# Performance work log

Measured on AMD Instinct MI355X. Metric: run time of the kernel, lower is better.

## Reference

```python
import jax, jax.numpy as jnp
import numpy as np

B, L, DM, E, N, R, S = 2, 1024, 512, 1024, 16, 32, 64
BN_SCALE = float(1.0 / np.sqrt(1.0 + 1e-5))  # eval-mode BatchNorm1d with default running stats


def _ssm(x, Wx, bx, Wdt, bdt, A_log, D):
    # x: [B,L,E] -> Mamba selective scan output [B,L,E]
    dbc = x @ Wx.T + bx                                   # [B,L,R+2N]
    delta = jax.nn.softplus(dbc[..., :R] @ Wdt.T + bdt)   # [B,L,E]
    Bm = dbc[..., R:R + N]                                # [B,L,N]
    Cm = dbc[..., R + N:]                                 # [B,L,N]
    A = -jnp.exp(A_log)                                   # [E,N]
    dA = jnp.exp(delta[..., None] * A)                    # [B,L,E,N]
    dBx = delta[..., None] * Bm[:, :, None, :] * x[..., None]

    def comb(c1, c2):
        a1, b1 = c1
        a2, b2 = c2
        return a1 * a2, b1 * a2 + b2

    _, h = jax.lax.associative_scan(comb, (dA, dBx), axis=1)  # [B,L,E,N]
    return jnp.einsum('blen,bln->ble', h, Cm) + D * x


def _gmask_idx(length, batch):
    ref = (length + 1) // 2
    idx = jnp.arange(length, dtype=jnp.float32)
    sigma = jnp.abs(idx - ref).mean()
    w = jnp.exp(-0.5 * (idx - ref) ** 2 / sigma ** 2)
    w = w / w.sum()
    return jnp.broadcast_to(w, (batch, length))


def _gmask_vec(seq):
    length = seq.shape[1]
    ref = seq[:, (length + 1) // 2, :]
    d = jnp.linalg.norm(seq - ref[:, None, :], axis=2)    # [B,L]
    sigma = d.mean(axis=1, keepdims=True)
    w = jnp.exp(-0.5 * (d / sigma) ** 2)
    return w / w.sum(axis=1, keepdims=True)


def _spatial_attn(x, w, b):
    # x: [B,L,C]; SpatialAttention: returns weighted map in [B,C,L] layout
    xt = jnp.swapaxes(x, 1, 2)                            # [B,C,L]
    fmap = (w[0] * xt.max(axis=1) + w[1] * xt.mean(axis=1) + b) * BN_SCALE
    wmap = jax.nn.sigmoid(jax.nn.relu(fmap))[:, None, :]  # [B,1,L]
    return xt * wmap                                      # [B,C,L]


def _forward(x, W_in_x, b_in_x, W_in_z, b_in_z, convf_w, convf_b, convb_w, convb_b,
             Wx_f, bx_f, Wdt_f, bdt_f, A_log_f, D_f,
             Wx_b, bx_b, Wdt_b, bdt_b, A_log_b, D_b,
             W_cat, b_cat, sa_w, sa_b, wA_f, wV_f,
             W_proj, b_proj, W_Bi, b_Bi, tf_w, tf_b, W_out, b_out):
    b_, l_, _ = x.shape
    xi = x @ W_in_x.T + b_in_x                            # [B,L,E]
    z = x @ W_in_z.T + b_in_z                             # [B,L,E]
    # depthwise conv1d with kernel_size=1 == per-channel affine
    x_f = jax.nn.silu(xi * convf_w + convf_b)
    x_b = jax.nn.silu(jnp.flip(xi, axis=1) * convb_w + convb_b)
    y_f = jnp.tanh(_ssm(x_f, Wx_f, bx_f, Wdt_f, bdt_f, A_log_f, D_f))
    y_b = jnp.tanh(_ssm(x_b, Wx_b, bx_b, Wdt_b, bdt_b, A_log_b, D_b))
    gi = _gmask_idx(l_, b_)
    mf = jax.nn.softmax(gi * _gmask_vec(y_f), axis=1)
    mb = jax.nn.softmax(gi * _gmask_vec(y_b), axis=1)
    y_cat = jnp.concatenate([y_f * mf[..., None],
                             y_b * jnp.flip(mb[..., None], axis=1)], axis=-1)
    y = y_cat @ W_cat.T + b_cat                           # [B,L,E]
    m = jax.nn.softmax(gi * _gmask_vec(y_cat), axis=1)
    y = y * m[..., None]
    yw = _spatial_attn(y, sa_w, sa_b)                     # [B,E,L]
    y = jnp.swapaxes(yw, 1, 2)                            # [B,L,E]
    # STL tokenizer (forward direction weights)
    Aw = jax.nn.softmax(jnp.swapaxes(y @ wA_f.T, 1, 2), axis=-1)  # [B,S,L]
    u = Aw @ (y @ wV_f)                                   # [B,S,E]
    # z branch: adaptive average pool L -> S (L % S == 0), then SiLU
    zp = jax.nn.silu(jnp.swapaxes(z, 1, 2).reshape(b_, E, S, l_ // S).mean(-1))
    zt = jnp.swapaxes(zp, 1, 2)                           # [B,S,E]
    # TokenFuser -- faithful to original's .view-based memory reinterpretation
    Y = (u.reshape(b_, E, S) @ W_proj.T + b_proj).reshape(b_, S, E)
    Bw = jax.nn.sigmoid(zt @ W_Bi.T + b_Bi)               # [B,S,S]
    BwY = Bw @ Y                                          # [B,S,E]
    xj = _spatial_attn(zt, tf_w, tf_b).reshape(b_, S, E)  # view (reshape), not transpose
    out = BwY + xj
    return jnp.tanh(out @ W_out.T + b_out)                # [B,S,DM]


def setup_inputs():
    ks = jax.random.split(jax.random.key(0), 24)
    g = lambda i, shape, s=0.02: jax.random.normal(ks[i], shape, dtype=jnp.float32) * s
    A_log = jnp.log(jnp.tile(jnp.arange(1, N + 1, dtype=jnp.float32), (E, 1)))
    return dict(
        x=jax.random.normal(ks[0], (B, L, DM), dtype=jnp.float32),
        W_in_x=g(1, (E, DM)), b_in_x=jnp.zeros((E,), jnp.float32),
        W_in_z=g(2, (E, DM)), b_in_z=jnp.zeros((E,), jnp.float32),
        convf_w=1.0 + g(3, (E,)), convf_b=jnp.zeros((E,), jnp.float32),
        convb_w=1.0 + g(4, (E,)), convb_b=jnp.zeros((E,), jnp.float32),
        Wx_f=g(5, (R + 2 * N, E)), bx_f=jnp.zeros((R + 2 * N,), jnp.float32),
        Wdt_f=g(6, (E, R)), bdt_f=jnp.full((E,), -4.0, jnp.float32),
        A_log_f=A_log, D_f=jnp.ones((E,), jnp.float32),
        Wx_b=g(7, (R + 2 * N, E)), bx_b=jnp.zeros((R + 2 * N,), jnp.float32),
        Wdt_b=g(8, (E, R)), bdt_b=jnp.full((E,), -4.0, jnp.float32),
        A_log_b=A_log, D_b=jnp.ones((E,), jnp.float32),
        W_cat=g(9, (E, 2 * E)), b_cat=jnp.zeros((E,), jnp.float32),
        sa_w=g(10, (2,), 0.5), sa_b=jnp.zeros((), jnp.float32),
        wA_f=g(11, (S, E), 0.05), wV_f=g(12, (E, E), 0.02),
        W_proj=g(13, (S, S), 0.1), b_proj=jnp.zeros((S,), jnp.float32),
        W_Bi=g(14, (S, E)), b_Bi=jnp.zeros((S,), jnp.float32),
        tf_w=g(15, (2,), 0.5), tf_b=jnp.zeros((), jnp.float32),
        W_out=g(16, (DM, E)), b_out=jnp.zeros((DM,), jnp.float32),
    )


def reference(x, W_in_x, b_in_x, W_in_z, b_in_z, convf_w, convf_b, convb_w, convb_b,
              Wx_f, bx_f, Wdt_f, bdt_f, A_log_f, D_f,
              Wx_b, bx_b, Wdt_b, bdt_b, A_log_b, D_b,
              W_cat, b_cat, sa_w, sa_b, wA_f, wV_f,
              W_proj, b_proj, W_Bi, b_Bi, tf_w, tf_b, W_out, b_out):
    return _forward(x, W_in_x, b_in_x, W_in_z, b_in_z, convf_w, convf_b, convb_w, convb_b,
                    Wx_f, bx_f, Wdt_f, bdt_f, A_log_f, D_f,
                    Wx_b, bx_b, Wdt_b, bdt_b, A_log_b, D_b,
                    W_cat, b_cat, sa_w, sa_b, wA_f, wV_f,
                    W_proj, b_proj, W_Bi, b_Bi, tf_w, tf_b, W_out, b_out)
```

## Files before the change

kernel.cpp:

```cpp
#include <hip/hip_runtime.h>
#include <math.h>

#define DEVI static __device__ __forceinline__

namespace {

constexpr float BN_SCALE_C = 0.9999950000374997f;

typedef __bf16 bf8v __attribute__((ext_vector_type(8)));
typedef float f4v __attribute__((ext_vector_type(4)));

DEVI float sigmoidf_(float x){ return 1.0f/(1.0f+expf(-x)); }
DEVI float siluf_(float x){ return x/(1.0f+expf(-x)); }
DEVI float softplusf_(float x){ return fmaxf(x,0.0f) + log1pf(__expf(-fabsf(x))); }

DEVI unsigned short f2bf(float f){
  union{float f; unsigned int u;} v; v.f=f;
  unsigned int r = v.u + 0x7fffu + ((v.u>>16)&1u);
  return (unsigned short)(r>>16);
}

DEVI float bredw_sum(float v, float* sh){
  #pragma unroll
  for (int o=32;o;o>>=1) v += __shfl_xor(v, o);
  __syncthreads();
  if ((threadIdx.x&63)==0) sh[threadIdx.x>>6] = v;
  __syncthreads();
  return sh[0]+sh[1]+sh[2]+sh[3];
}
DEVI float bredw_max(float v, float* sh){
  #pragma unroll
  for (int o=32;o;o>>=1) v = fmaxf(v, __shfl_xor(v, o));
  __syncthreads();
  if ((threadIdx.x&63)==0) sh[threadIdx.x>>6] = v;
  __syncthreads();
  return fmaxf(fmaxf(sh[0],sh[1]), fmaxf(sh[2],sh[3]));
}

DEVI void gld_lds16(const unsigned short* g, unsigned short* l){
  __builtin_amdgcn_global_load_lds(
      (const __attribute__((address_space(1))) unsigned int*)(g),
      (__attribute__((address_space(3))) unsigned int*)(l), 16, 0, 0);
}

DEVI void stage_tile64(const unsigned short* __restrict__ Ak,
                       const unsigned short* __restrict__ Bk,
                       size_t lda, size_t ldb,
                       unsigned short* As, unsigned short* Bs,
                       int w, int lane)
{
  #pragma unroll
  for (int i=0;i<2;++i){
    int seg = (w<<1) + i;
    int row = (seg<<3) + (lane>>3);
    int c   = (lane & 7) ^ (row & 7);
    gld_lds16(Ak + (size_t)row*lda + (c<<3), As + (seg<<9));
    gld_lds16(Bk + (size_t)row*ldb + (c<<3), Bs + (seg<<9));
  }
}

DEVI void gemm_core(const unsigned short* __restrict__ Ag,
                    const unsigned short* __restrict__ Bg,
                    size_t lda, size_t ldb, int ksteps,
                    unsigned short* As, unsigned short* Bs, f4v (&acc)[2][2])
{
  const int tid = threadIdx.x;
  const int lane = tid & 63, w = tid >> 6;
  const int wr = w >> 1, wc = w & 1;
  const int l15 = lane & 15, l4 = lane >> 4;

  int cur = 0;
  stage_tile64(Ag, Bg, lda, ldb, As, Bs, w, lane);
  asm volatile("s_waitcnt vmcnt(0)" ::: "memory");
  __syncthreads();
  for (int ks = 0; ks < ksteps; ++ks){
    unsigned short* Asc = As + (cur<<12);
    unsigned short* Bsc = Bs + (cur<<12);
    if (ks+1 < ksteps)
      stage_tile64(Ag + (size_t)(ks+1)*64, Bg + (size_t)(ks+1)*64, lda, ldb,
                   As + ((cur^1)<<12), Bs + ((cur^1)<<12), w, lane);
    #pragma unroll
    for (int kk=0;kk<2;++kk){
      int cb = (kk<<2) + l4;
      bf8v af[2], bfv[2];
      #pragma unroll
      for (int mi=0;mi<2;++mi){
        int row = (wr<<5)+(mi<<4)+l15;
        af[mi] = *(const bf8v*)(Asc + (row<<6) + ((cb^(row&7))<<3));
      }
      #pragma unroll
      for (int ni=0;ni<2;++ni){
        int row = (wc<<5)+(ni<<4)+l15;
        bfv[ni] = *(const bf8v*)(Bsc + (row<<6) + ((cb^(row&7))<<3));
      }
      #pragma unroll
      for (int mi=0;mi<2;++mi)
        #pragma unroll
        for (int ni=0;ni<2;++ni)
          acc[mi][ni] = __builtin_amdgcn_mfma_f32_16x16x32_bf16(af[mi], bfv[ni], acc[mi][ni], 0,0,0);
    }
    asm volatile("s_waitcnt vmcnt(0)" ::: "memory");
    __syncthreads();
    cur ^= 1;
  }
}

template<int EPI>
__global__ __launch_bounds__(256) void gemm_bf16_k(
    const unsigned short* __restrict__ A, const unsigned short* __restrict__ Bt,
    const float* __restrict__ bias, void* __restrict__ Cout,
    int N, int K,
    const unsigned short* __restrict__ Bt2, const float* __restrict__ bias2, long sC)
{
  __shared__ unsigned short As[8192], Bs[8192];
  float* Cf = (float*)Cout;
  if (Bt2 && blockIdx.z){ Bt = Bt2; bias = bias2; Cf += sC; }
  const int m0 = blockIdx.y<<6, n0 = blockIdx.x<<6;
  f4v acc[2][2] = {};
  gemm_core(A + (size_t)m0*K, Bt + (size_t)n0*K, K, K, K>>6, As, Bs, acc);
  const int lane = threadIdx.x & 63, w = threadIdx.x >> 6;
  const int wr = w>>1, wc = w&1, l15 = lane&15, l4 = lane>>4;
  #pragma unroll
  for (int mi=0;mi<2;++mi)
    #pragma unroll
    for (int ni=0;ni<2;++ni){
      int col = n0 + (wc<<5) + (ni<<4) + l15;
      float bv = bias ? bias[col] : 0.f;
      #pragma unroll
      for (int r=0;r<4;++r){
        int rowg = m0 + (wr<<5) + (mi<<4) + (l4<<2) + r;
        Cf[(size_t)rowg*N + col] = acc[mi][ni][r] + bv;
      }
    }
}

template<int EPI>
__global__ __launch_bounds__(256) void gemm_small_k(
    const unsigned short* __restrict__ A, const unsigned short* __restrict__ Bt,
    const float* __restrict__ b0, const float* __restrict__ b1,
    void* __restrict__ Cout, int N, int K, int mshift, long sB)
{
  __shared__ unsigned char smem[65536];
  unsigned short* AsAll = (unsigned short*)smem;
  unsigned short* BsAll = (unsigned short*)(smem + 32768);
  float* Lc = (float*)smem;

  const int tid = threadIdx.x;
  const int lane = tid & 63, w = tid >> 6;
  const int m0 = blockIdx.y<<6, n0 = blockIdx.x<<6;
  const unsigned short* Ab = A + (size_t)m0*K;
  const unsigned short* Bb = Bt + (size_t)(m0>>mshift)*sB + (size_t)n0*K;
  unsigned short* Asw = AsAll + (w<<12);
  unsigned short* Bsw = BsAll + (w<<12);
  const int kpw = K >> 2;
  const int nst = kpw >> 6;
  const int l15 = lane & 15, l4 = lane >> 4;
  const int srow8 = lane >> 3, sc = lane & 7;

  f4v acc[4][4] = {};
  for (int ks = 0; ks < nst; ++ks){
    const int kbase = w*kpw + (ks<<6);
    #pragma unroll
    for (int seg=0; seg<8; ++seg){
      int row = (seg<<3) + srow8;
      int c = sc ^ (row & 7);
      gld_lds16(Ab + (size_t)row*K + kbase + (c<<3), Asw + (seg<<9));
      gld_lds16(Bb + (size_t)row*K + kbase + (c<<3), Bsw + (seg<<9));
    }
    asm volatile("s_waitcnt vmcnt(0)" ::: "memory");
    #pragma unroll
    for (int kk=0; kk<2; ++kk){
      int cb = (kk<<2) + l4;
      bf8v af[4], bfv[4];
      #pragma unroll
      for (int mi=0;mi<4;++mi){
        int row = (mi<<4) + l15;
        af[mi] = *(const bf8v*)(Asw + (row<<6) + ((cb^(row&7))<<3));
      }
      #pragma unroll
      for (int ni=0;ni<4;++ni){
        int row = (ni<<4) + l15;
        bfv[ni] = *(const bf8v*)(Bsw + (row<<6) + ((cb^(row&7))<<3));
      }
      #pragma unroll
      for (int mi=0;mi<4;++mi)
        #pragma unroll
        for (int ni=0;ni<4;++ni)
          acc[mi][ni] = __builtin_amdgcn_mfma_f32_16x16x32_bf16(af[mi], bfv[ni], acc[mi][ni], 0,0,0);
    }
    __builtin_amdgcn_sched_barrier(0);
  }
  __syncthreads();
  #pragma unroll
  for (int mi=0;mi<4;++mi)
    #pragma unroll
    for (int ni=0;ni<4;++ni){
      int col = (ni<<4) + l15;
      #pragma unroll
      for (int r=0;r<4;++r){
        int row = (mi<<4) + (l4<<2) + r;
        Lc[(w<<12) + (row<<6) + col] = acc[mi][ni][r];
      }
    }
  __syncthreads();
  {
    const int basei = tid << 4;
    const int row = basei >> 6, colb = basei & 63;
    float vals[16];
    #pragma unroll
    for (int q=0;q<4;++q){
      float4 a0 = *(const float4*)(Lc + basei + (q<<2));
      float4 a1 = *(const float4*)(Lc + 4096 + basei + (q<<2));
      float4 a2 = *(const float4*)(Lc + 8192 + basei + (q<<2));
      float4 a3 = *(const float4*)(Lc + 12288 + basei + (q<<2));
      vals[(q<<2)+0] = a0.x+a1.x+a2.x+a3.x;
      vals[(q<<2)+1] = a0.y+a1.y+a2.y+a3.y;
      vals[(q<<2)+2] = a0.z+a1.z+a2.z+a3.z;
      vals[(q<<2)+3] = a0.w+a1.w+a2.w+a3.w;
    }
    if (EPI==1){
      unsigned short* Cb = (unsigned short*)Cout + (size_t)(m0+row)*N + n0 + colb;
      union{unsigned short u[16]; uint4 q[2];} o;
      #pragma unroll
      for (int j=0;j<16;++j) o.u[j] = f2bf(vals[j]);
      *(uint4*)(Cb) = o.q[0];
      *(uint4*)(Cb+8) = o.q[1];
    } else {
      const float* bias = (b1 && (m0>>mshift)) ? b1 : b0;
      float* Cb = (float*)Cout + (size_t)(m0+row)*N + n0 + colb;
      #pragma unroll
      for (int q=0;q<4;++q){
        float4 v;
        float* vp = &v.x;
        #pragma unroll
        for (int j=0;j<4;++j){
          float t = vals[(q<<2)+j] + (bias ? bias[n0+colb+(q<<2)+j] : 0.f);
          if (EPI==2) t = tanhf(t);
          vp[j] = t;
        }
        *(float4*)(Cb + (q<<2)) = v;
      }
    }
  }
}

__global__ __launch_bounds__(256) void castall_k(
    const float* __restrict__ s0, unsigned short* __restrict__ d0, int n0,
    const float* __restrict__ s1, unsigned short* __restrict__ d1, int n1,
    const float* __restrict__ s2, unsigned short* __restrict__ d2, int n2,
    const float* __restrict__ s3, unsigned short* __restrict__ d3, int n3,
    const float* __restrict__ s4, unsigned short* __restrict__ d4, int n4,
    const float* __restrict__ s5, unsigned short* __restrict__ d5, int n5,
    const float* __restrict__ s6, unsigned short* __restrict__ d6, int n6,
    const float* __restrict__ s7, unsigned short* __restrict__ d7, int n7,
    const float* __restrict__ wV, unsigned short* __restrict__ wVT,
    const float* __restrict__ Wdt_f, const float* __restrict__ Wdt_b,
    float* __restrict__ WdtT)
{
  __shared__ float tsh[32][33];
  if (blockIdx.x >= 4800){
    int tb = blockIdx.x - 4800;
    int tx = threadIdx.x & 31, ty = threadIdx.x >> 5;
    if (tb < 1024){
      int by = tb >> 5, bx = tb & 31;
      #pragma unroll
      for (int r=0;r<4;++r){
        int row = by*32 + ty + r*8;
        tsh[ty + r*8][tx] = wV[(long)row*1024 + bx*32 + tx];
      }
      __syncthreads();
      #pragma unroll
      for (int r=0;r<4;++r){
        int row = bx*32 + ty + r*8;
        wVT[(long)row*1024 + by*32 + tx] = f2bf(tsh[tx][ty + r*8]);
      }
    } else {
      int q = tb - 1024;
      int dir = q >> 5, bi = q & 31;
      const float* src = dir ? Wdt_b : Wdt_f;
      float* dst = WdtT + (dir<<15);
      #pragma unroll
      for (int r=0;r<4;++r){
        int row = bi*32 + ty + r*8;
        tsh[ty + r*8][tx] = src[(long)row*32 + tx];
      }
      __syncthreads();
      #pragma unroll
      for (int r=0;r<4;++r){
        int c = ty + r*8;
        dst[(long)c*1024 + bi*32 + tx] = tsh[tx][c];
      }
    }
    return;
  }
  int i = (blockIdx.x*256 + threadIdx.x)*4;
  const float* s; unsigned short* d;
  if (i < n0){ s = s0; d = d0; }
  else if ((i -= n0) < n1){ s = s1; d = d1; }
  else if ((i -= n1) < n2){ s = s2; d = d2; }
  else if ((i -= n2) < n3){ s = s3; d = d3; }
  else if ((i -= n3) < n4){ s = s4; d = d4; }
  else if ((i -= n4) < n5){ s = s5; d = d5; }
  else if ((i -= n5) < n6){ s = s6; d = d6; }
  else if ((i -= n6) < n7){ s = s7; d = d7; }
  else return;
  float4 v = *(const float4*)(s + i);
  union{ unsigned short u[4]; uint2 p; } o;
  o.u[0]=f2bf(v.x); o.u[1]=f2bf(v.y); o.u[2]=f2bf(v.z); o.u[3]=f2bf(v.w);
  *(uint2*)(d + i) = o.p;
}

__global__ __launch_bounds__(256) void convzt_k(const float* __restrict__ xi, const float* __restrict__ z,
    const float* __restrict__ cfw, const float* __restrict__ cfb,
    const float* __restrict__ cbw, const float* __restrict__ cbb,
    float* __restrict__ xf, float* __restrict__ xb, unsigned short* __restrict__ xfb_bf,
    float* __restrict__ ztb)
{
  int bx = blockIdx.x, t = threadIdx.x;
  if (bx < 2048){
    int base = (bx*256 + t) << 2;
    int e = base & 1023;
    int bl = base >> 10; int l = bl & 1023, b = bl >> 10;
    float4 cw = *(const float4*)(cfw + e);
    float4 cb = *(const float4*)(cfb + e);
    float4 xv = *(const float4*)(xi + base);
    float4 vf;
    vf.x = siluf_(fmaf(xv.x, cw.x, cb.x));
    vf.y = siluf_(fmaf(xv.y, cw.y, cb.y));
    vf.z = siluf_(fmaf(xv.z, cw.z, cb.z));
    vf.w = siluf_(fmaf(xv.w, cw.w, cb.w));
    *(float4*)(xf + base) = vf;
    union{unsigned short u[4]; uint2 p;} o;
    o.u[0]=f2bf(vf.x); o.u[1]=f2bf(vf.y); o.u[2]=f2bf(vf.z); o.u[3]=f2bf(vf.w);
    *(uint2*)(xfb_bf + base) = o.p;
    int jb = (((b<<10) + (1023-l))<<10) + e;
    float4 cw2 = *(const float4*)(cbw + e);
    float4 cb2 = *(const float4*)(cbb + e);
    float4 xw = *(const float4*)(xi + jb);
    float4 vb;
    vb.x = siluf_(fmaf(xw.x, cw2.x, cb2.x));
    vb.y = siluf_(fmaf(xw.y, cw2.y, cb2.y));
    vb.z = siluf_(fmaf(xw.z, cw2.z, cb2.z));
    vb.w = siluf_(fmaf(xw.w, cw2.w, cb2.w));
    *(float4*)(xb + base) = vb;
    union{unsigned short u[4]; uint2 p;} o2;
    o2.u[0]=f2bf(vb.x); o2.u[1]=f2bf(vb.y); o2.u[2]=f2bf(vb.z); o2.u[3]=f2bf(vb.w);
    *(uint2*)(xfb_bf + 2097152 + base) = o2.p;
  } else {
    int base = ((bx-2048)*256 + t) << 2;
    int e = base & 1023; int bs = base >> 10; int s = bs & 63; int b = bs >> 6;
    const float* zp = z + (((long)((b<<10)+(s<<4)))<<10) + e;
    float4 sm = {0.f,0.f,0.f,0.f};
    #pragma unroll
    for (int j=0;j<16;++j){
      float4 v = *(const float4*)(zp + ((long)j<<10));
      sm.x += v.x; sm.y += v.y; sm.z += v.z; sm.w += v.w;
    }
    float4 o;
    o.x = siluf_(sm.x*(1.f/16.f)); o.y = siluf_(sm.y*(1.f/16.f));
    o.z = siluf_(sm.z*(1.f/16.f)); o.w = siluf_(sm.w*(1.f/16.f));
    *(float4*)(ztb + base) = o;
  }
}

__global__ __launch_bounds__(256) void ssm_chunk_k(
    const float* __restrict__ xs0, const float* __restrict__ dbc0,
    const float* __restrict__ A_log_f, const float* __restrict__ A_log_b,
    const float* __restrict__ WdtT,
    const float* __restrict__ bdt_f, const float* __restrict__ bdt_b,
    float* __restrict__ pA0, float* __restrict__ hend0)
{
  const int dir = blockIdx.y;
  const float* xs   = xs0  + (size_t)dir*2097152;
  const float* dbc  = dbc0 + (size_t)dir*131072;
  const float* A_log= dir ? A_log_b : A_log_f;
  float* pA   = pA0   + (size_t)dir*1048576;
  float* hend = hend0 + (size_t)dir*1048576;

  __shared__ float sB[32][16];
  __shared__ float sD[32][32];
  int g = blockIdx.x*256 + threadIdx.x;
  int e = g & 1023;
  int bc = g >> 10;
  int c = bc & 31, b = bc >> 5;
  for (int i=threadIdx.x; i<512; i+=256){
    int l=i>>4, n=i&15;
    sB[l][n] = dbc[(((b<<10) + (c<<5) + l)<<6) + 32 + n];
  }
  for (int i=threadIdx.x; i<1024; i+=256){
    int l=i>>5, k=i&31;
    sD[l][k] = dbc[(((b<<10) + (c<<5) + l)<<6) + k];
  }
  __syncthreads();
  float wdt[32];
  {
    const float* WT = WdtT + (dir<<15) + e;
    #pragma unroll
    for (int k=0;k<32;++k) wdt[k] = WT[(size_t)k<<10];
  }
  const float bde = (dir ? bdt_b : bdt_f)[e];
  float An[16];
  #pragma unroll
  for (int n=0;n<16;++n) An[n] = -__expf(A_log[(e<<4)+n]);
  float h[16], p[16];
  #pragma unroll
  for (int n=0;n<16;++n){ h[n]=0.0f; p[n]=1.0f; }
  long base = ((long)((b<<10) + (c<<5)))*1024 + e;
  for (int l=0;l<32;++l){
    float accd = bde;
    #pragma unroll
    for (int k=0;k<32;++k) accd = fmaf(sD[l][k], wdt[k], accd);
    float dl = softplusf_(accd);
    float xv = xs[base + ((long)l<<10)];
    float dx = dl*xv;
    #pragma unroll
    for (int n=0;n<16;++n){
      float a = __expf(dl*An[n]);
      h[n] = fmaf(a, h[n], dx*sB[l][n]);
      p[n] *= a;
    }
  }
  long ob = ((long)((b<<5)+c)<<4)*1024 + e;
  #pragma unroll
  for (int n=0;n<16;++n){ pA[ob + ((long)n<<10)] = p[n]; hend[ob + ((long)n<<10)] = h[n]; }
}

__global__ __launch_bounds__(256) void ssm_carry_k(
    const float* __restrict__ pA, const float* __restrict__ hend, float* __restrict__ Hc)
{
  int i = blockIdx.x*256 + threadIdx.x;
  int e = i & 1023, n = (i>>10)&15, b = (i>>14)&1, dir = (i>>15)&1;
  const float* pAd = pA   + (size_t)dir*1048576;
  const float* hd  = hend + (size_t)dir*1048576;
  float* Hd        = Hc   + (size_t)dir*1048576;
  float H = 0.f;
  long base = ((long)(b*512 + n))*1024 + e;
  for (int c=0;c<32;++c){
    long a = base + (long)c*16384;
    Hd[a] = H;
    H = fmaf(pAd[a], H, hd[a]);
  }
}

__global__ __launch_bounds__(256) void ssm_out_k(
    const float* __restrict__ xs0, const float* __restrict__ dbc0,
    const float* __restrict__ A_log_f, const float* __restrict__ A_log_b,
    const float* __restrict__ WdtT,
    const float* __restrict__ bdt_f, const float* __restrict__ bdt_b,
    const float* __restrict__ Hc0,
    const float* __restrict__ D_f, const float* __restrict__ D_b,
    float* __restrict__ y0)
{
  const int dir = blockIdx.y;
  const float* xs   = xs0  + (size_t)dir*2097152;
  const float* dbc  = dbc0 + (size_t)dir*131072;
  const float* A_log= dir ? A_log_b : A_log_f;
  const float* Hc   = Hc0 + (size_t)dir*1048576;
  const float* D    = dir ? D_b : D_f;
  float* y          = y0 + (size_t)dir*2097152;

  __shared__ float sB[32][16], sC[32][16];
  __shared__ float sD[32][32];
  int g = blockIdx.x*256+threadIdx.x;
  int e = g & 1023;
  int bc = g >> 10;
  int c = bc & 31, b = bc >> 5;
  for (int i=threadIdx.x;i<512;i+=256){
    int l=i>>4, n=i&15;
    int base = ((b<<10)+(c<<5)+l)<<6;
    sB[l][n] = dbc[base+32+n];
    sC[l][n] = dbc[base+48+n];
  }
  for (int i=threadIdx.x; i<1024; i+=256){
    int l=i>>5, k=i&31;
    sD[l][k] = dbc[(((b<<10) + (c<<5) + l)<<6) + k];
  }
  __syncthreads();
  float wdt[32];
  {
    const float* WT = WdtT + (dir<<15) + e;
    #pragma unroll
    for (int k=0;k<32;++k) wdt[k] = WT[(size_t)k<<10];
  }
  const float bde = (dir ? bdt_b : bdt_f)[e];
  float An[16], h[16];
  long ib = ((long)((b<<5)+c)<<4)*1024 + e;
  #pragma unroll
  for(int n=0;n<16;++n){ An[n] = -__expf(A_log[(e<<4)+n]); h[n]=Hc[ib+((long)n<<10)]; }
  float Dv = D[e];
  long base = ((long)((b<<10)+(c<<5)))*1024 + e;
  for (int l=0;l<32;++l){
    float accd = bde;
    #pragma unroll
    for (int k=0;k<32;++k) accd = fmaf(sD[l][k], wdt[k], accd);
    float dl = softplusf_(accd);
    float xv = xs[base+((long)l<<10)];
    float dx = dl*xv;
    float acc = Dv*xv;
    #pragma unroll
    for(int n=0;n<16;++n){
      float a = __expf(dl*An[n]);
      h[n] = fmaf(a,h[n],dx*sB[l][n]);
      acc = fmaf(h[n], sC[l][n], acc);
    }
    y[base+((long)l<<10)] = tanhf(acc);
  }
}

__global__ __launch_bounds__(256) void stats_k(const float* __restrict__ y,
    float* __restrict__ nrm, float* __restrict__ dotv)
{
  __shared__ float sh[4];
  int row = blockIdx.x;
  int rowref = (row & ~1023) + 512;
  const float4* rp  = (const float4*)(y + (long)row*1024);
  const float4* rf  = (const float4*)(y + (long)rowref*1024);
  float4 a = rp[threadIdx.x], r = rf[threadIdx.x];
  float sn = a.x*a.x + a.y*a.y + a.z*a.z + a.w*a.w;
  float sd = a.x*r.x + a.y*r.y + a.z*r.z + a.w*r.w;
  sn = bredw_sum(sn, sh);
  sd = bredw_sum(sd, sh);
  if (threadIdx.x==0){ nrm[row] = sn; dotv[row] = sd; }
}

DEVI void softmask(const float (&d)[4], const float (&gi)[4], float gsum,
                   float* sh, float (&m)[4])
{
  float s = d[0]+d[1]+d[2]+d[3];
  float sig = bredw_sum(s, sh) * (1.0f/1024.0f);
  float inv = 1.0f/sig;
  float w[4]; s = 0.f;
  #pragma unroll
  for (int i=0;i<4;++i){ float r = d[i]*inv; w[i] = __expf(-0.5f*r*r); s += w[i]; }
  float wsm = bredw_sum(s, sh);
  float sc = 1.0f/(wsm*gsum);
  float tv[4]; float mx = -1e30f;
  #pragma unroll
  for (int i=0;i<4;++i){ tv[i] = gi[i]*w[i]*sc; mx = fmaxf(mx, tv[i]); }
  mx = bredw_max(mx, sh);
  s = 0.f;
  #pragma unroll
  for (int i=0;i<4;++i){ tv[i] = __expf(tv[i]-mx); s += tv[i]; }
  float es = bredw_sum(s, sh);
  float ie = 1.0f/es;
  #pragma unroll
  for (int i=0;i<4;++i) m[i] = tv[i]*ie;
}

__global__ __launch_bounds__(256) void mask2_k(
    const float* __restrict__ nrm, const float* __restrict__ dotv,
    float* __restrict__ mfG, float* __restrict__ mbG, float* __restrict__ mvG)
{
  __shared__ float mfs[1024], mbs[1024], sh[4];
  const int b = blockIdx.x, t = threadIdx.x;
  const float nf512 = nrm[(b<<10)+512];
  const float nb512 = nrm[2048+(b<<10)+512];
  float gi[4], nf[4], pf[4], nb[4], pb[4];
  float gs = 0.f;
  #pragma unroll
  for (int i=0;i<4;++i){
    int l = t + (i<<8);
    float q = (float)(l-512) * (1.0f/256.0f);
    gi[i] = __expf(-0.5f*q*q); gs += gi[i];
    nf[i] = nrm[(b<<10)+l];      pf[i] = dotv[(b<<10)+l];
    nb[i] = nrm[2048+(b<<10)+l]; pb[i] = dotv[2048+(b<<10)+l];
  }
  float gsum = bredw_sum(gs, sh);
  float mf[4], mb[4], d[4];
  #pragma unroll
  for (int i=0;i<4;++i) d[i] = sqrtf(fmaxf(nf[i] - 2.f*pf[i] + nf512, 0.f));
  softmask(d, gi, gsum, sh, mf);
  #pragma unroll
  for (int i=0;i<4;++i) d[i] = sqrtf(fmaxf(nb[i] - 2.f*pb[i] + nb512, 0.f));
  softmask(d, gi, gsum, sh, mb);
  #pragma unroll
  for (int i=0;i<4;++i){
    int l = t + (i<<8);
    mfs[l] = mf[i]; mbs[l] = mb[i];
    mfG[(b<<10)+l] = mf[i]; mbG[(b<<10)+l] = mb[i];
  }
  __syncthreads();
  const float mf512 = mfs[512], mb511 = mbs[511];
  #pragma unroll
  for (int i=0;i<4;++i){
    int l = t + (i<<8);
    float mbf = mbs[1023-l];
    float dc2 = mf[i]*mf[i]*nf[i] - 2.f*mf[i]*mf512*pf[i] + mf512*mf512*nf512
              + mbf*mbf*nb[i]     - 2.f*mbf*mb511*pb[i]   + mb511*mb511*nb512;
    d[i] = sqrtf(fmaxf(dc2, 0.f));
  }
  float mv[4];
  softmask(d, gi, gsum, sh, mv);
  #pragma unroll
  for (int i=0;i<4;++i) mvG[(b<<10)+t+(i<<8)] = mv[i];
}

__global__ __launch_bounds__(256) void ycat_k(const float* __restrict__ yf, const float* __restrict__ yb,
    const float* __restrict__ mf, const float* __restrict__ mb, unsigned short* __restrict__ yc)
{
  int base = (blockIdx.x*256 + threadIdx.x) << 2;
  int e = base & 1023; int bl = base >> 10; int l = bl & 1023, b = bl >> 10;
  float mfv = mf[bl];
  float mbv = mb[(b<<10) + (1023-l)];
  float4 vf = *(const float4*)(yf + base);
  float4 vb = *(const float4*)(yb + base);
  long r = (long)bl*2048;
  union{unsigned short u[4]; uint2 p;} o;
  o.u[0]=f2bf(vf.x*mfv); o.u[1]=f2bf(vf.y*mfv); o.u[2]=f2bf(vf.z*mfv); o.u[3]=f2bf(vf.w*mfv);
  *(uint2*)(yc + r + e) = o.p;
  union{unsigned short u[4]; uint2 p;} o2;
  o2.u[0]=f2bf(vb.x*mbv); o2.u[1]=f2bf(vb.y*mbv); o2.u[2]=f2bf(vb.z*mbv); o2.u[3]=f2bf(vb.w*mbv);
  *(uint2*)(yc + r + 1024 + e) = o2.p;
}

__global__ __launch_bounds__(256) void rowscale_k(const float* __restrict__ y, const float* __restrict__ m,
    const float* __restrict__ sw, const float* __restrict__ sb, unsigned short* __restrict__ yo)
{
  __shared__ float sh[4];
  int row = blockIdx.x;
  float mv = m[row];
  float4 v = ((const float4*)(y + (long)row*1024))[threadIdx.x];
  v.x *= mv; v.y *= mv; v.z *= mv; v.w *= mv;
  float mx = fmaxf(fmaxf(v.x,v.y), fmaxf(v.z,v.w));
  float sm = v.x+v.y+v.z+v.w;
  float rmax = bredw_max(mx, sh);
  float rsum = bredw_sum(sm, sh);
  float fmap = (sw[0]*rmax + sw[1]*(rsum*(1.0f/1024.0f)) + sb[0])*BN_SCALE_C;
  float sc = sigmoidf_(fmaxf(fmap, 0.0f));
  union{unsigned short u[4]; uint2 p;} o;
  o.u[0]=f2bf(v.x*sc); o.u[1]=f2bf(v.y*sc); o.u[2]=f2bf(v.z*sc); o.u[3]=f2bf(v.w*sc);
  *(uint2*)(yo + (long)row*1024 + (threadIdx.x<<2)) = o.p;
}

__global__ __launch_bounds__(256) void awsmT_k(const float* __restrict__ yA,
    unsigned short* __restrict__ Aw,
    const unsigned short* __restrict__ src, unsigned short* __restrict__ dst)
{
  __shared__ float sh[4];
  __shared__ unsigned short tsh[32][33];
  if (blockIdx.x < 128){
    int bs = blockIdx.x; int b = bs >> 6, s = bs & 63;
    float v[4]; float mx=-1e30f;
    #pragma unroll
    for(int i=0;i<4;++i){
      int l = threadIdx.x+(i<<8);
      v[i] = yA[(long)((b<<10)+l)*64 + s];
      mx = fmaxf(mx, v[i]);
    }
    mx = bredw_max(mx, sh);
    float sm=0.0f;
    #pragma unroll
    for(int i=0;i<4;++i){ v[i]=__expf(v[i]-mx); sm+=v[i]; }
    sm = bredw_sum(sm, sh);
    float inv = 1.0f/sm;
    #pragma unroll
    for(int i=0;i<4;++i){ int l=threadIdx.x+(i<<8); Aw[(((b<<6)+s)<<10)+l] = f2bf(v[i]*inv); }
  } else {
    int tb = blockIdx.x - 128;
    size_t bo = (size_t)(tb>>10) << 20;
    int rem = tb & 1023;
    int by = rem >> 5, bx = rem & 31;
    int tx = threadIdx.x & 31, ty = threadIdx.x >> 5;
    #pragma unroll
    for (int r=0;r<4;++r){
      int row = by*32 + ty + r*8;
      tsh[ty + r*8][tx] = src[bo + (long)row*1024 + bx*32 + tx];
    }
    __syncthreads();
    #pragma unroll
    for (int r=0;r<4;++r){
      int row = bx*32 + ty + r*8;
      dst[bo + (long)row*1024 + by*32 + tx] = tsh[tx][ty + r*8];
    }
  }
}

__global__ __launch_bounds__(256) void upbw_k(const float* __restrict__ u2f,
    const float* __restrict__ W_proj, const float* __restrict__ b_proj,
    const float* __restrict__ zt, const float* __restrict__ W_Bi,
    const float* __restrict__ b_Bi, const float* __restrict__ tw,
    const float* __restrict__ tb,
    float* __restrict__ Yp, float* __restrict__ Bw, float* __restrict__ gz)
{
  __shared__ float a[1024];
  __shared__ float sh[4];
  const int t = threadIdx.x;
  if (blockIdx.x < 256){
    const int r0 = blockIdx.x*8;
    for (int idx=t; idx<512; idx+=256){
      int r = idx>>6, sp = idx&63;
      a[idx] = u2f[(long)(r0+r)*64 + sp];
    }
    __syncthreads();
    int r = t >> 5, c = t & 31;
    const float* ar = a + (r<<6);
    float acc1 = b_proj[c], acc2 = b_proj[c+32];
    for (int sp=0; sp<64; ++sp){
      float av = ar[sp];
      acc1 = fmaf(av, W_proj[c*64+sp], acc1);
      acc2 = fmaf(av, W_proj[(c+32)*64+sp], acc2);
    }
    long row = r0 + r;
    Yp[row*64 + c] = acc1;
    Yp[row*64 + c + 32] = acc2;
  } else {
    const int row = blockIdx.x - 256;
    float4 zv = ((const float4*)(zt + (long)row*1024))[t];
    *(float4*)(a + (t<<2)) = zv;
    float mx = fmaxf(fmaxf(zv.x,zv.y), fmaxf(zv.z,zv.w));
    float sm = zv.x+zv.y+zv.z+zv.w;
    mx = bredw_max(mx, sh);
    sm = bredw_sum(sm, sh);
    if (t==0){
      float f = (tw[0]*mx + tw[1]*(sm*(1.0f/1024.0f)) + tb[0])*BN_SCALE_C;
      gz[row] = sigmoidf_(fmaxf(f,0.0f));
    }
    __syncthreads();
    int col = t >> 2, q = t & 3;
    const float4* wp = (const float4*)(W_Bi + (long)col*1024 + q*256);
    const float4* zp = (const float4*)(a + q*256);
    float acc = 0.f;
    for (int i=0;i<64;++i){
      float4 w = wp[i], zc = zp[i];
      acc += w.x*zc.x + w.y*zc.y + w.z*zc.z + w.w*zc.w;
    }
    acc += __shfl_xor(acc, 1);
    acc += __shfl_xor(acc, 2);
    if (q==0) Bw[(long)row*64 + col] = sigmoidf_(acc + b_Bi[col]);
  }
}

__global__ __launch_bounds__(256) void o_k(const float* __restrict__ Bw,
    const float* __restrict__ Yp, const float* __restrict__ zt,
    const float* __restrict__ gz, unsigned short* __restrict__ O_bf)
{
  __shared__ float bwrow[64];
  const int t = threadIdx.x;
  const int bs = blockIdx.x; const int b = bs >> 6, s = bs & 63;
  if (t < 64) bwrow[t] = Bw[(long)bs*64 + t];
  __syncthreads();
  const int e0 = t << 2;
  const float* yb = Yp + (long)b*65536 + e0;
  float4 acc = {0.f,0.f,0.f,0.f};
  for (int s2=0; s2<64; ++s2){
    float f = bwrow[s2];
    float4 y = *(const float4*)(yb + ((long)s2<<10));
    acc.x = fmaf(f,y.x,acc.x); acc.y = fmaf(f,y.y,acc.y);
    acc.z = fmaf(f,y.z,acc.z); acc.w = fmaf(f,y.w,acc.w);
  }
  int ez = (s<<4) + (e0>>6);
  float o4[4] = {acc.x, acc.y, acc.z, acc.w};
  union{unsigned short u[4]; uint2 p;} o;
  #pragma unroll
  for (int k=0;k<4;++k){
    int sz = (e0&63) + k;
    float xj = zt[(((long)((b<<6)+sz))<<10) + ez] * gz[(b<<6)+sz];
    o.u[k] = f2bf(o4[k] + xj);
  }
  *(uint2*)(O_bf + (long)bs*1024 + e0) = o.p;
}

}

extern "C" void kernel_launch(void* const* d_in, const int* in_sizes, int n_in,
                              void* d_out, int out_size, void* d_ws, size_t ws_size,
                              hipStream_t stream)
{
  (void)in_sizes; (void)n_in; (void)out_size; (void)ws_size;
  const float* x      = (const float*)d_in[0];
  const float* W_in_x = (const float*)d_in[1];
  const float* b_in_x = (const float*)d_in[2];
  const float* W_in_z = (const float*)d_in[3];
  const float* b_in_z = (const float*)d_in[4];
  const float* cfw    = (const float*)d_in[5];
  const float* cfb    = (const float*)d_in[6];
  const float* cbw    = (const float*)d_in[7];
  const float* cbb    = (const float*)d_in[8];
  const float* Wx_f   = (const float*)d_in[9];
  const float* bx_f   = (const float*)d_in[10];
  const float* Wdt_f  = (const float*)d_in[11];
  const float* bdt_f  = (const float*)d_in[12];
  const float* A_log_f= (const float*)d_in[13];
  const float* D_f    = (const float*)d_in[14];
  const float* Wx_b   = (const float*)d_in[15];
  const float* bx_b   = (const float*)d_in[16];
  const float* Wdt_b  = (const float*)d_in[17];
  const float* bdt_b  = (const float*)d_in[18];
  const float* A_log_b= (const float*)d_in[19];
  const float* D_b    = (const float*)d_in[20];
  const float* W_cat  = (const float*)d_in[21];
  const float* b_cat  = (const float*)d_in[22];
  const float* sa_w   = (const float*)d_in[23];
  const float* sa_b   = (const float*)d_in[24];
  const float* wA_f   = (const float*)d_in[25];
  const float* wV_f   = (const float*)d_in[26];
  const float* W_proj = (const float*)d_in[27];
  const float* b_proj = (const float*)d_in[28];
  const float* W_Bi   = (const float*)d_in[29];
  const float* b_Bi   = (const float*)d_in[30];
  const float* tf_w   = (const float*)d_in[31];
  const float* tf_b   = (const float*)d_in[32];
  const float* W_out  = (const float*)d_in[33];
  const float* b_out  = (const float*)d_in[34];
  float* out = (float*)d_out;
  float* ws  = (float*)d_ws;

  const size_t M1 = 1u<<20;
  float* xi = ws;
  float* pA = ws;
  unsigned short* ycat_bf = (unsigned short*)ws;
  float* z = ws + 2*M1;
  float* hend = ws + 2*M1;
  float* ybufF = ws + 2*M1;
  float* xf = ws + 4*M1;
  unsigned short* ybuf_bf = (unsigned short*)(ws + 4*M1);
  float* xb = ws + 6*M1;
  unsigned short* ybufT_bf = (unsigned short*)(ws + 6*M1);
  float* yf = ws + 8*M1;
  float* yb = ws + 10*M1;
  float* u2f = ws + 10*M1;
  unsigned short* xfxb_bf = (unsigned short*)(ws + 12*M1);
  unsigned short* x_bf = (unsigned short*)(ws + 17*M1);
  float* Hc = ws + 16*M1;
  float* dbcF = ws + 18*M1;
  size_t woff = 18*M1 + 262144;
  unsigned short* Winx_bf = (unsigned short*)(ws + woff); woff += 262144;
  unsigned short* Winz_bf = (unsigned short*)(ws + woff); woff += 262144;
  unsigned short* Wcat_bf = (unsigned short*)(ws + woff); woff += M1;
  unsigned short* wVT_bf  = (unsigned short*)(ws + woff); woff += 524288;
  unsigned short* wA_bf   = (unsigned short*)(ws + woff); woff += 32768;
  unsigned short* Wx_bf   = (unsigned short*)(ws + woff); woff += 65536;
  unsigned short* Wout_bf = (unsigned short*)(ws + woff); woff += 262144;
  float* WdtT = ws + woff; woff += 65536;
  float* ztb  = ws + woff; woff += 131072;
  float* nrm  = ws + woff; woff += 4096;
  float* dotv = ws + woff; woff += 4096;
  float* mfG  = ws + woff; woff += 2048;
  float* mbG  = ws + woff; woff += 2048;
  float* mvG  = ws + woff; woff += 2048;
  float* gz   = ws + woff; woff += 256;
  float* yA   = ws + woff; woff += 131072;
  unsigned short* Aw_bf = (unsigned short*)(ws + woff); woff += 65536;
  unsigned short* uR_bf = (unsigned short*)(ws + woff); woff += 65536;
  float* Yp   = ws + woff; woff += 131072;
  float* Bw   = ws + woff; woff += 8192;
  unsigned short* O_bf = (unsigned short*)(ws + woff); woff += 65536;

  dim3 blk(256);

  castall_k<<<5888,blk,0,stream>>>(x, x_bf, 1048576,
                                   W_in_x, Winx_bf, 524288,
                                   W_in_z, Winz_bf, 524288,
                                   W_cat, Wcat_bf, 2097152,
                                   wA_f, wA_bf, 65536,
                                   Wx_f, Wx_bf, 65536,
                                   Wx_b, Wx_bf + 65536, 65536,
                                   W_out, Wout_bf, 524288,
                                   wV_f, wVT_bf, Wdt_f, Wdt_b, WdtT);

  gemm_bf16_k<0><<<dim3(16,32,2),blk,0,stream>>>(x_bf, Winx_bf, b_in_x, xi, 1024, 512,
                                                 Winz_bf, b_in_z, (long)(2*M1));
  convzt_k<<<2176,blk,0,stream>>>(xi, z, cfw,cfb,cbw,cbb, xf, xb, xfxb_bf, ztb);

  gemm_small_k<0><<<dim3(1,64),blk,0,stream>>>(xfxb_bf, Wx_bf, bx_f, bx_b, dbcF,
                                               64, 1024, 11, 65536);

  ssm_chunk_k<<<dim3(256,2),blk,0,stream>>>(xf, dbcF, A_log_f, A_log_b,
                                            WdtT, bdt_f, bdt_b, pA, hend);
  ssm_carry_k<<<256,blk,0,stream>>>(pA, hend, Hc);
  ssm_out_k<<<dim3(256,2),blk,0,stream>>>(xf, dbcF, A_log_f, A_log_b,
                                          WdtT, bdt_f, bdt_b, Hc, D_f, D_b, yf);

  stats_k<<<4096,blk,0,stream>>>(yf, nrm, dotv);
  mask2_k<<<2,blk,0,stream>>>(nrm, dotv, mfG, mbG, mvG);
  ycat_k<<<2048,blk,0,stream>>>(yf, yb, mfG, mbG, ycat_bf);

  gemm_bf16_k<0><<<dim3(16,32,1),blk,0,stream>>>(ycat_bf, Wcat_bf, b_cat, ybufF, 1024, 2048,
                                                 nullptr, nullptr, 0);
  rowscale_k<<<2048,blk,0,stream>>>(ybufF, mvG, sa_w, sa_b, ybuf_bf);

  gemm_small_k<0><<<dim3(1,32),blk,0,stream>>>(ybuf_bf, wA_bf, nullptr, nullptr, yA,
                                               64, 1024, 31, 0);
  awsmT_k<<<2176,blk,0,stream>>>(yA, Aw_bf, ybuf_bf, ybufT_bf);
  gemm_small_k<1><<<dim3(16,2),blk,0,stream>>>(Aw_bf, ybufT_bf, nullptr, nullptr, uR_bf,
                                               1024, 1024, 6, (long)M1);
  gemm_small_k<0><<<dim3(16,2),blk,0,stream>>>(uR_bf, wVT_bf, nullptr, nullptr, u2f,
                                               1024, 1024, 31, 0);

  upbw_k<<<384,blk,0,stream>>>(u2f, W_proj, b_proj, ztb, W_Bi, b_Bi, tf_w, tf_b, Yp, Bw, gz);
  o_k<<<128,blk,0,stream>>>(Bw, Yp, ztb, gz, O_bf);

  gemm_small_k<2><<<dim3(8,2),blk,0,stream>>>(O_bf, Wout_bf, b_out, nullptr, out,
                                              512, 1024, 31, 0);
}
```

Measured before the change: 217.7 us.

## Precompute SSM delta in separate kernel and split state dim across half-waves

Adds a dbcdelta_k kernel that computes softplus(dt-projection) once into a workspace buffer, so the chunk and output scan kernels no longer each redo the 32-term dot product and softplus per timestep. The scan kernels now split the 16 state channels across two half-waves (8 each), doubling the grid and reducing per-thread registers, with a shuffle to combine output partial sums. The chunk decay product is computed as exp(sum(delta)*A) instead of a running product. This trades extra global traffic for the delta buffer and an extra launch against less redundant compute and higher occupancy.

```diff
diff --git a/kernel.cpp b/kernel.cpp
--- a/kernel.cpp
+++ b/kernel.cpp
@@ -363,66 +363,100 @@
   }
 }
 
+__global__ __launch_bounds__(256) void dbcdelta_k(
+    const float* __restrict__ dbcF, const float* __restrict__ WdtT,
+    const float* __restrict__ bdt_f, const float* __restrict__ bdt_b,
+    float* __restrict__ delta)
+{
+  __shared__ float sdbc[8][64];
+  const int t = threadIdx.x;
+  const int r0 = blockIdx.x * 8;
+  const int dir = r0 >> 11;
+  const float* bdt = dir ? bdt_b : bdt_f;
+  const float* WT  = WdtT + (dir<<15);
+  for (int idx=t; idx<512; idx+=256){
+    int r = idx>>6, c = idx&63;
+    sdbc[r][c] = dbcF[(long)(r0+r)*64 + c];
+  }
+  __syncthreads();
+  const int c0 = t << 2;
+  float4 bv = *(const float4*)(bdt + c0);
+  float4 acc[8];
+  #pragma unroll
+  for (int r=0;r<8;++r) acc[r] = bv;
+  #pragma unroll
+  for (int k=0;k<32;++k){
+    float4 w = *(const float4*)(WT + (k<<10) + c0);
+    #pragma unroll
+    for (int r=0;r<8;++r){
+      float a = sdbc[r][k];
+      acc[r].x = fmaf(a, w.x, acc[r].x);
+      acc[r].y = fmaf(a, w.y, acc[r].y);
+      acc[r].z = fmaf(a, w.z, acc[r].z);
+      acc[r].w = fmaf(a, w.w, acc[r].w);
+    }
+  }
+  #pragma unroll
+  for (int r=0;r<8;++r){
+    float4 o;
+    o.x = softplusf_(acc[r].x); o.y = softplusf_(acc[r].y);
+    o.z = softplusf_(acc[r].z); o.w = softplusf_(acc[r].w);
+    *(float4*)(delta + (long)(r0+r)*1024 + c0) = o;
+  }
+}
+
 __global__ __launch_bounds__(256) void ssm_chunk_k(
-    const float* __restrict__ xs0, const float* __restrict__ dbc0,
-    const float* __restrict__ A_log_f, const float* __restrict__ A_log_b,
-    const float* __restrict__ WdtT,
-    const float* __restrict__ bdt_f, const float* __restrict__ bdt_b,
+    const float* __restrict__ xs0, const float* __restrict__ dl0,
+    const float* __restrict__ dbc0, const float* __restrict__ A_log_f,
+    const float* __restrict__ A_log_b,
     float* __restrict__ pA0, float* __restrict__ hend0)
 {
   const int dir = blockIdx.y;
   const float* xs   = xs0  + (size_t)dir*2097152;
+  const float* delta= dl0  + (size_t)dir*2097152;
   const float* dbc  = dbc0 + (size_t)dir*131072;
   const float* A_log= dir ? A_log_b : A_log_f;
   float* pA   = pA0   + (size_t)dir*1048576;
   float* hend = hend0 + (size_t)dir*1048576;
 
   __shared__ float sB[32][16];
-  __shared__ float sD[32][32];
-  int g = blockIdx.x*256 + threadIdx.x;
-  int e = g & 1023;
-  int bc = g >> 10;
-  int c = bc & 31, b = bc >> 5;
-  for (int i=threadIdx.x; i<512; i+=256){
+  const int tid = threadIdx.x;
+  const int lane = tid & 63, w = tid >> 6;
+  const int le = lane & 31, half = lane >> 5;
+  const int bc = blockIdx.x >> 3;
+  const int b = bc >> 5, c = bc & 31;
+  const int e = ((blockIdx.x & 7) << 7) + (w << 5) + le;
+  for (int i=tid; i<512; i+=256){
     int l=i>>4, n=i&15;
     sB[l][n] = dbc[(((b<<10) + (c<<5) + l)<<6) + 32 + n];
   }
-  for (int i=threadIdx.x; i<1024; i+=256){
-    int l=i>>5, k=i&31;
-    sD[l][k] = dbc[(((b<<10) + (c<<5) + l)<<6) + k];
-  }
-  __syncthreads();
-  float wdt[32];
-  {
-    const float* WT = WdtT + (dir<<15) + e;
-    #pragma unroll
-    for (int k=0;k<32;++k) wdt[k] = WT[(size_t)k<<10];
-  }
-  const float bde = (dir ? bdt_b : bdt_f)[e];
-  float An[16];
-  #pragma unroll
-  for (int n=0;n<16;++n) An[n] = -__expf(A_log[(e<<4)+n]);
-  float h[16], p[16];
-  #pragma unroll
-  for (int n=0;n<16;++n){ h[n]=0.0f; p[n]=1.0f; }
+  __syncthreads();
+  const int n0 = half << 3;
+  float An[8];
+  #pragma unroll
+  for (int j=0;j<8;++j) An[j] = -__expf(A_log[(e<<4)+n0+j]);
+  float h[8];
+  #pragma unroll
+  for (int j=0;j<8;++j) h[j]=0.0f;
+  float ds = 0.f;
   long base = ((long)((b<<10) + (c<<5)))*1024 + e;
   for (int l=0;l<32;++l){
-    float accd = bde;
-    #pragma unroll
-    for (int k=0;k<32;++k) accd = fmaf(sD[l][k], wdt[k], accd);
-    float dl = softplusf_(accd);
+    float dl = delta[base + ((long)l<<10)];
     float xv = xs[base + ((long)l<<10)];
     float dx = dl*xv;
-    #pragma unroll
-    for (int n=0;n<16;++n){
-      float a = __expf(dl*An[n]);
-      h[n] = fmaf(a, h[n], dx*sB[l][n]);
-      p[n] *= a;
+    ds += dl;
+    #pragma unroll
+    for (int j=0;j<8;++j){
+      float a = __expf(dl*An[j]);
+      h[j] = fmaf(a, h[j], dx*sB[l][n0+j]);
     }
   }
   long ob = ((long)((b<<5)+c)<<4)*1024 + e;
   #pragma unroll
-  for (int n=0;n<16;++n){ pA[ob + ((long)n<<10)] = p[n]; hend[ob + ((long)n<<10)] = h[n]; }
+  for (int j=0;j<8;++j){
+    pA[ob + ((long)(n0+j)<<10)] = __expf(ds*An[j]);
+    hend[ob + ((long)(n0+j)<<10)] = h[j];
+  }
 }
 
 __global__ __launch_bounds__(256) void ssm_carry_k(
@@ -443,16 +477,15 @@
 }
 
 __global__ __launch_bounds__(256) void ssm_out_k(
-    const float* __restrict__ xs0, const float* __restrict__ dbc0,
-    const float* __restrict__ A_log_f, const float* __restrict__ A_log_b,
-    const float* __restrict__ WdtT,
-    const float* __restrict__ bdt_f, const float* __restrict__ bdt_b,
-    const float* __restrict__ Hc0,
+    const float* __restrict__ xs0, const float* __restrict__ dl0,
+    const float* __restrict__ dbc0, const float* __restrict__ A_log_f,
+    const float* __restrict__ A_log_b, const float* __restrict__ Hc0,
     const float* __restrict__ D_f, const float* __restrict__ D_b,
     float* __restrict__ y0)
 {
   const int dir = blockIdx.y;
   const float* xs   = xs0  + (size_t)dir*2097152;
+  const float* delta= dl0  + (size_t)dir*2097152;
   const float* dbc  = dbc0 + (size_t)dir*131072;
   const float* A_log= dir ? A_log_b : A_log_f;
   const float* Hc   = Hc0 + (size_t)dir*1048576;
@@ -460,50 +493,42 @@
   float* y          = y0 + (size_t)dir*2097152;
 
   __shared__ float sB[32][16], sC[32][16];
-  __shared__ float sD[32][32];
-  int g = blockIdx.x*256+threadIdx.x;
-  int e = g & 1023;
-  int bc = g >> 10;
-  int c = bc & 31, b = bc >> 5;
-  for (int i=threadIdx.x;i<512;i+=256){
+  const int tid = threadIdx.x;
+  const int lane = tid & 63, w = tid >> 6;
+  const int le = lane & 31, half = lane >> 5;
+  const int bc = blockIdx.x >> 3;
+  const int b = bc >> 5, c = bc & 31;
+  const int e = ((blockIdx.x & 7) << 7) + (w << 5) + le;
+  for (int i=tid;i<512;i+=256){
     int l=i>>4, n=i&15;
-    int base = ((b<<10)+(c<<5)+l)<<6;
-    sB[l][n] = dbc[base+32+n];
-    sC[l][n] = dbc[base+48+n];
-  }
-  for (int i=threadIdx.x; i<1024; i+=256){
-    int l=i>>5, k=i&31;
-    sD[l][k] = dbc[(((b<<10) + (c<<5) + l)<<6) + k];
-  }
-  __syncthreads();
-  float wdt[32];
-  {
-    const float* WT = WdtT + (dir<<15) + e;
-    #pragma unroll
-    for (int k=0;k<32;++k) wdt[k] = WT[(size_t)k<<10];
-  }
-  const float bde = (dir ? bdt_b : bdt_f)[e];
-  float An[16], h[16];
+    int bbase = ((b<<10)+(c<<5)+l)<<6;
+    sB[l][n] = dbc[bbase+32+n];
+    sC[l][n] = dbc[bbase+48+n];
+  }
+  __syncthreads();
+  const int n0 = half << 3;
+  float An[8], h[8];
   long ib = ((long)((b<<5)+c)<<4)*1024 + e;
   #pragma unroll
-  for(int n=0;n<16;++n){ An[n] = -__expf(A_log[(e<<4)+n]); h[n]=Hc[ib+((long)n<<10)]; }
-  float Dv = D[e];
+  for(int j=0;j<8;++j){
+    An[j] = -__expf(A_log[(e<<4)+n0+j]);
+    h[j] = Hc[ib+((long)(n0+j)<<10)];
+  }
+  const float Dv = D[e];
   long base = ((long)((b<<10)+(c<<5)))*1024 + e;
   for (int l=0;l<32;++l){
-    float accd = bde;
-    #pragma unroll
-    for (int k=0;k<32;++k) accd = fmaf(sD[l][k], wdt[k], accd);
-    float dl = softplusf_(accd);
+    float dl = delta[base+((long)l<<10)];
     float xv = xs[base+((long)l<<10)];
     float dx = dl*xv;
-    float acc = Dv*xv;
-    #pragma unroll
-    for(int n=0;n<16;++n){
-      float a = __expf(dl*An[n]);
-      h[n] = fmaf(a,h[n],dx*sB[l][n]);
-      acc = fmaf(h[n], sC[l][n], acc);
-    }
-    y[base+((long)l<<10)] = tanhf(acc);
+    float acc = half ? 0.f : Dv*xv;
+    #pragma unroll
+    for(int j=0;j<8;++j){
+      float a = __expf(dl*An[j]);
+      h[j] = fmaf(a,h[j],dx*sB[l][n0+j]);
+      acc = fmaf(h[j], sC[l][n0+j], acc);
+    }
+    acc += __shfl_xor(acc, 32);
+    if (!half) y[base+((long)l<<10)] = tanhf(acc);
   }
 }
 
@@ -820,6 +845,7 @@
   float* yb = ws + 10*M1;
   float* u2f = ws + 10*M1;
   unsigned short* xfxb_bf = (unsigned short*)(ws + 12*M1);
+  float* deltaF = ws + 12*M1;
   unsigned short* x_bf = (unsigned short*)(ws + 17*M1);
   float* Hc = ws + 16*M1;
   float* dbcF = ws + 18*M1;
@@ -864,12 +890,11 @@
 
   gemm_small_k<0><<<dim3(1,64),blk,0,stream>>>(xfxb_bf, Wx_bf, bx_f, bx_b, dbcF,
                                                64, 1024, 11, 65536);
-
-  ssm_chunk_k<<<dim3(256,2),blk,0,stream>>>(xf, dbcF, A_log_f, A_log_b,
-                                            WdtT, bdt_f, bdt_b, pA, hend);
+  dbcdelta_k<<<512,blk,0,stream>>>(dbcF, WdtT, bdt_f, bdt_b, deltaF);
+
+  ssm_chunk_k<<<dim3(512,2),blk,0,stream>>>(xf, deltaF, dbcF, A_log_f, A_log_b, pA, hend);
   ssm_carry_k<<<256,blk,0,stream>>>(pA, hend, Hc);
-  ssm_out_k<<<dim3(256,2),blk,0,stream>>>(xf, dbcF, A_log_f, A_log_b,
-                                          WdtT, bdt_f, bdt_b, Hc, D_f, D_b, yf);
+  ssm_out_k<<<dim3(512,2),blk,0,stream>>>(xf, deltaF, dbcF, A_log_f, A_log_b, Hc, D_f, D_b, yf);
 
   stats_k<<<4096,blk,0,stream>>>(yf, nrm, dotv);
   mask2_k<<<2,blk,0,stream>>>(nrm, dotv, mfG, mbG, mvG);
```

Result: faster. 209.8 us (-3.6%).
